# Kernel optimization log

Measured on AMD Instinct MI355X. Metric: run time of the kernel, lower is better.

Reference implementation:

```python
import jax, jax.numpy as jnp
import numpy as np

B, S, D, H = 4, 2048, 768, 8
HD = D // H
EPS = 1e-5
NEG = -1e9


def setup_inputs() -> dict:
    key = jax.random.key(0)
    ks = jax.random.split(key, 12)
    s = 1.0 / np.sqrt(D)
    inp = {
        "hidden_states": jax.random.normal(ks[0], (B, S, D), dtype=jnp.float32),
        "anchor_mask": jax.random.bernoulli(ks[1], 0.5, (B, S)),
        "ln_g": jnp.ones((D,), jnp.float32),
        "ln_b": jnp.zeros((D,), jnp.float32),
        "Wq": jax.random.uniform(ks[2], (D, D), jnp.float32, -s, s),
        "bq": jax.random.uniform(ks[3], (D,), jnp.float32, -s, s),
        "Wk": jax.random.uniform(ks[4], (D, D), jnp.float32, -s, s),
        "bk": jax.random.uniform(ks[5], (D,), jnp.float32, -s, s),
        "Wv": jax.random.uniform(ks[6], (D, D), jnp.float32, -s, s),
        "bv": jax.random.uniform(ks[7], (D,), jnp.float32, -s, s),
        "Wo": jax.random.uniform(ks[8], (D, D), jnp.float32, -s, s),
        "bo": jax.random.uniform(ks[9], (D,), jnp.float32, -s, s),
    }
    return inp


def reference(hidden_states, anchor_mask, ln_g, ln_b, Wq, bq, Wk, bk, Wv, bv, Wo, bo):
    # LayerNorm (per-token, so applying to all tokens == applying to gathered anchors)
    mu = jnp.mean(hidden_states, axis=-1, keepdims=True)
    var = jnp.mean(jnp.square(hidden_states - mu), axis=-1, keepdims=True)
    x = (hidden_states - mu) * jax.lax.rsqrt(var + EPS) * ln_g + ln_b

    # QKV projections: torch Linear is x @ W.T + b
    q = (jnp.einsum('bsd,ed->bse', x, Wq) + bq).reshape(B, S, H, HD)
    k = (jnp.einsum('bsd,ed->bse', x, Wk) + bk).reshape(B, S, H, HD)
    v = (jnp.einsum('bsd,ed->bse', x, Wv) + bv).reshape(B, S, H, HD)

    scale = 1.0 / np.sqrt(HD)
    scores = jnp.einsum('bqhd,bkhd->bhqk', q, k) * scale
    # keys restricted to anchor positions (equivalent to the gather)
    key_mask = anchor_mask[:, None, None, :]  # (B,1,1,S)
    scores = jnp.where(key_mask, scores, NEG)
    attn = jax.nn.softmax(scores, axis=-1)  # dropout is identity in eval

    out = jnp.einsum('bhqk,bkhd->bqhd', attn, v).reshape(B, S, D)
    out = jnp.einsum('bsd,ed->bse', out, Wo) + bo
    # scatter back: zeros at non-anchor positions
    return out * anchor_mask[:, :, None].astype(out.dtype)
```

## Files before the change

### kernel.cpp

```cpp
#include <hip/hip_runtime.h>
#include <math.h>

#define S_LEN 2048
#define D_DIM 768
#define NH 8
#define HD 96
#define NTOK 8192

typedef short bf16x8 __attribute__((ext_vector_type(8)));
typedef float f32x4 __attribute__((ext_vector_type(4)));
typedef float f32x16 __attribute__((ext_vector_type(16)));
typedef unsigned int u32x2 __attribute__((ext_vector_type(2)));
typedef unsigned int u32x4 __attribute__((ext_vector_type(4)));

__device__ __forceinline__ f32x4 mfma16(bf16x8 a, bf16x8 b, f32x4 c) {
    return __builtin_amdgcn_mfma_f32_16x16x32_bf16(a, b, c, 0, 0, 0);
}
__device__ __forceinline__ f32x16 mfma32(bf16x8 a, bf16x8 b, f32x16 c) {
    return __builtin_amdgcn_mfma_f32_32x32x16_bf16(a, b, c, 0, 0, 0);
}

__device__ __forceinline__ unsigned short f2bf(float f) {
    unsigned int u = __float_as_uint(f);
    u += 0x7fffu + ((u >> 16) & 1u);
    return (unsigned short)(u >> 16);
}

__device__ __forceinline__ unsigned int cvtpk(float lo, float hi) {
    unsigned int r;
    asm("v_cvt_pk_bf16_f32 %0, %1, %2" : "=v"(r) : "v"(lo), "v"(hi));
    return r;
}

__device__ __forceinline__ void gl_lds16(const unsigned short* g, unsigned short* l) {
    __builtin_amdgcn_global_load_lds(
        (const __attribute__((address_space(1))) unsigned int*)g,
        (__attribute__((address_space(3))) unsigned int*)l, 16, 0, 0);
}

#define TILE_SHORTS 6144
#define BH_SHORTS   196608

__global__ __launch_bounds__(256) void prep_kernel(
    const unsigned char* __restrict__ mb, int* __restrict__ idx, int* __restrict__ cnt,
    const float* __restrict__ Wq, const float* __restrict__ Wk,
    const float* __restrict__ Wv, const float* __restrict__ Wo,
    unsigned short* __restrict__ W4b, float* __restrict__ out)
{
    const int bi = blockIdx.x;
    const int t  = threadIdx.x;

    if (bi < 4) {
        __shared__ int red[4];
        __shared__ int warp_tot[4];
        const int b = bi;
        int s = 0;
        for (int i = t; i < NTOK; i += 256) s += (int)mb[i];
        for (int off = 32; off > 0; off >>= 1) s += __shfl_down(s, off, 64);
        if ((t & 63) == 0) red[t >> 6] = s;
        __syncthreads();
        const int total = red[0] + red[1] + red[2] + red[3];
        const int mode = (total > 20000) ? 2 : ((total > 2500) ? 1 : 0);
        const int*   mi = (const int*)mb;
        const float* mf = (const float*)mb;
        const int p0 = t * 8;
        int av = 0, c = 0;
        #pragma unroll
        for (int j = 0; j < 8; ++j) {
            const int g = b * S_LEN + p0 + j;
            bool a;
            if (mode == 2)      a = (mf[g] != 0.0f);
            else if (mode == 1) a = (mb[g] != 0);
            else                a = (mi[g] != 0);
            if (a) { av |= (1 << j); ++c; }
        }
        const int lane = t & 63, w = t >> 6;
        int v = c;
        #pragma unroll
        for (int off = 1; off < 64; off <<= 1) {
            const int u = __shfl_up(v, off, 64);
            if (lane >= off) v += u;
        }
        if (lane == 63) warp_tot[w] = v;
        __syncthreads();
        int wbase = 0;
        for (int i = 0; i < w; ++i) wbase += warp_tot[i];
        int o = wbase + v - c;
        #pragma unroll
        for (int j = 0; j < 8; ++j)
            if (av & (1 << j)) idx[b * S_LEN + (o++)] = p0 + j;
        if (t == 255) cnt[b] = wbase + v;
    } else if (bi < 1156) {
        const int i = bi - 4;
        const int w = i / 288, blk = i % 288;
        const float* src = (w == 0) ? Wq : (w == 1) ? Wk : (w == 2) ? Wv : Wo;
        const int base = (blk * 256 + t) * 8;
        const float4 a = *(const float4*)&src[base];
        const float4 c = *(const float4*)&src[base + 4];
        uint4 u;
        u.x = (unsigned int)f2bf(a.x) | ((unsigned int)f2bf(a.y) << 16);
        u.y = (unsigned int)f2bf(a.z) | ((unsigned int)f2bf(a.w) << 16);
        u.z = (unsigned int)f2bf(c.x) | ((unsigned int)f2bf(c.y) << 16);
        u.w = (unsigned int)f2bf(c.z) | ((unsigned int)f2bf(c.w) << 16);
        *(uint4*)&W4b[(size_t)w * 589824 + base] = u;
    } else {
        const size_t i4 = (size_t)(bi - 1156) * 256 + t;
        float4 z; z.x = z.y = z.z = z.w = 0.0f;
        *(float4*)&out[i4 * 4] = z;
    }
}

__global__ __launch_bounds__(256) void ln_gather_kernel(
    const float* __restrict__ H, const float* __restrict__ g,
    const float* __restrict__ bta, const int* __restrict__ idx,
    const int* __restrict__ cnt, unsigned short* __restrict__ X)
{
    __shared__ float rs[4], rss[4];
    const int slot = blockIdx.x;
    const int b = slot >> 11, r = slot & (S_LEN - 1);
    if (r >= cnt[b]) return;
    const int p = idx[slot];
    const float* hr = H + (size_t)(b * S_LEN + p) * D_DIM;
    unsigned short* xr = X + (size_t)slot * D_DIM;
    const int t = threadIdx.x;
    const float v0 = hr[t], v1 = hr[t + 256], v2 = hr[t + 512];
    float s  = v0 + v1 + v2;
    float ss = v0*v0 + v1*v1 + v2*v2;
    for (int off = 32; off > 0; off >>= 1) {
        s  += __shfl_down(s,  off, 64);
        ss += __shfl_down(ss, off, 64);
    }
    if ((t & 63) == 0) { rs[t >> 6] = s; rss[t >> 6] = ss; }
    __syncthreads();
    const float sum = rs[0] + rs[1] + rs[2] + rs[3];
    const float sq  = rss[0] + rss[1] + rss[2] + rss[3];
    const float mu  = sum * (1.0f / D_DIM);
    const float var = sq * (1.0f / D_DIM) - mu * mu;
    const float rstd = rsqrtf(var + 1e-5f);
    xr[t]       = f2bf((v0 - mu) * rstd * g[t]       + bta[t]);
    xr[t + 256] = f2bf((v1 - mu) * rstd * g[t + 256] + bta[t + 256]);
    xr[t + 512] = f2bf((v2 - mu) * rstd * g[t + 512] + bta[t + 512]);
}

__global__ __launch_bounds__(256) void gemm_bf16(
    const unsigned short* __restrict__ A,
    const unsigned short* __restrict__ W4,
    const float* __restrict__ b0, const float* __restrict__ b1,
    const float* __restrict__ b2,
    const int* __restrict__ cnt, const int* __restrict__ idx,
    unsigned short* __restrict__ Qo, unsigned short* __restrict__ Kp,
    unsigned short* __restrict__ Vp, float* __restrict__ Fo,
    int oproj)
{
    const int z = blockIdx.z;
    const int m0 = blockIdx.y * 128;
    const int b  = m0 >> 11;
    const int rbase = m0 & (S_LEN - 1);
    const int nc = cnt[b];
    if (rbase >= nc) return;
    const int n0 = blockIdx.x * 128;
    const unsigned short* W = W4 + (size_t)z * 589824;
    const float* bias = (z == 0) ? b0 : (z == 1 ? b1 : b2);

    __shared__ unsigned short Al[128 * 32];
    __shared__ unsigned short Bl[128 * 32];

    const int t = threadIdx.x;
    const int srow = t >> 2, sg = t & 3;
    const int ra0 = b * S_LEN + min(rbase + srow,      nc - 1);
    const int ra1 = b * S_LEN + min(rbase + srow + 64, nc - 1);
    const unsigned short* gA0 = A + (size_t)ra0 * 768 + sg * 8;
    const unsigned short* gA1 = A + (size_t)ra1 * 768 + sg * 8;
    const unsigned short* gB0 = W + (size_t)(n0 + srow)      * 768 + sg * 8;
    const unsigned short* gB1 = W + (size_t)(n0 + srow + 64) * 768 + sg * 8;
    unsigned short* lA = Al + t * 8;
    unsigned short* lB = Bl + t * 8;

    const int w = t >> 6, lane = t & 63;
    const int l15 = lane & 15, quad = lane >> 4;
    const int mh = (w & 1) * 64, nh2 = (w >> 1) * 64;

    f32x4 acc[4][4] = {};

    int aoff[4], boff[4];
    #pragma unroll
    for (int i = 0; i < 4; ++i) {
        aoff[i] = (mh  + i * 16 + l15) * 32 + quad * 8;
        boff[i] = (nh2 + i * 16 + l15) * 32 + quad * 8;
    }

    for (int k0 = 0; k0 < 768; k0 += 32) {
        __syncthreads();
        gl_lds16(gA0 + k0, lA);
        gl_lds16(gA1 + k0, lA + 2048);
        gl_lds16(gB0 + k0, lB);
        gl_lds16(gB1 + k0, lB + 2048);
        __syncthreads();
        bf16x8 af[4], bfr[4];
        #pragma unroll
        for (int i = 0; i < 4; ++i) af[i]  = *(const bf16x8*)(Al + aoff[i]);
        #pragma unroll
        for (int i = 0; i < 4; ++i) bfr[i] = *(const bf16x8*)(Bl + boff[i]);
        #pragma unroll
        for (int ms = 0; ms < 4; ++ms)
            #pragma unroll
            for (int ns = 0; ns < 4; ++ns)
                acc[ms][ns] = mfma16(af[ms], bfr[ns], acc[ms][ns]);
    }

    if (!oproj) {
        if (z == 0) {
            #pragma unroll
            for (int ns = 0; ns < 4; ++ns) {
                const int n = n0 + nh2 + ns * 16 + l15;
                const float bv = bias[n];
                #pragma unroll
                for (int ms = 0; ms < 4; ++ms) {
                    const int ml = mh + ms * 16 + quad * 4;
                    #pragma unroll
                    for (int r = 0; r < 4; ++r) {
                        const int slot = b * S_LEN + rbase + ml + r;
                        Qo[(size_t)slot * 768 + n] = f2bf(acc[ms][ns][r] + bv);
                    }
                }
            }
        } else if (z == 1) {
            #pragma unroll
            for (int ns = 0; ns < 4; ++ns) {
                const int n = n0 + nh2 + ns * 16 + l15;
                const int h = n / 96, d = n - h * 96;
                const float bv = bias[n];
                unsigned short* base = Kp + (size_t)(b * 8 + h) * BH_SHORTS;
                const int dseg = d >> 3, dlo = d & 7;
                #pragma unroll
                for (int ms = 0; ms < 4; ++ms) {
                    const int ml = mh + ms * 16 + quad * 4;
                    #pragma unroll
                    for (int r = 0; r < 4; ++r) {
                        const int tok = rbase + ml + r;
                        const int kt = tok >> 6, tk = tok & 63;
                        const int g16 = tk >> 4, lr = tk & 15;
                        base[(size_t)kt * TILE_SHORTS +
                             (g16 * 192 + dseg * 16 + lr) * 8 + dlo] =
                            (tok < nc) ? f2bf(acc[ms][ns][r] + bv)
                                       : (unsigned short)0;
                    }
                }
            }
        } else {
            #pragma unroll
            for (int ns = 0; ns < 4; ++ns) {
                const int n = n0 + nh2 + ns * 16 + l15;
                const int h = n / 96, d = n - h * 96;
                const float bv = bias[n];
                unsigned short* base = Vp + (size_t)(b * 8 + h) * BH_SHORTS;
                const int dg = d >> 4, l16 = d & 15;
                #pragma unroll
                for (int ms = 0; ms < 4; ++ms) {
                    const int ml = mh + ms * 16 + quad * 4;
                    const int k = rbase + ml;
                    const int kt = k >> 6, tk = k & 63;
                    const int kseg = tk >> 3, klo = tk & 7;
                    const unsigned short h0 =
                        (k + 0 < nc) ? f2bf(acc[ms][ns][0] + bv) : (unsigned short)0;
                    const unsigned short h1 =
                        (k + 1 < nc) ? f2bf(acc[ms][ns][1] + bv) : (unsigned short)0;
                    const unsigned short h2 =
                        (k + 2 < nc) ? f2bf(acc[ms][ns][2] + bv) : (unsigned short)0;
                    const unsigned short h3 =
                        (k + 3 < nc) ? f2bf(acc[ms][ns][3] + bv) : (unsigned short)0;
                    uint2 u;
                    u.x = (unsigned int)h0 | ((unsigned int)h1 << 16);
                    u.y = (unsigned int)h2 | ((unsigned int)h3 << 16);
                    *(uint2*)&base[(size_t)kt * TILE_SHORTS +
                                   (dg * 128 + kseg * 16 + l16) * 8 + klo] = u;
                }
            }
        }
    } else {
        #pragma unroll
        for (int ns = 0; ns < 4; ++ns) {
            const int n = n0 + nh2 + ns * 16 + l15;
            const float bv = bias[n];
            #pragma unroll
            for (int ms = 0; ms < 4; ++ms) {
                const int ml = mh + ms * 16 + quad * 4;
                #pragma unroll
                for (int r = 0; r < 4; ++r) {
                    const int rloc = rbase + ml + r;
                    if (rloc < nc) {
                        const int orow = b * S_LEN + idx[b * S_LEN + rloc];
                        Fo[(size_t)orow * 768 + n] = acc[ms][ns][r] + bv;
                    }
                }
            }
        }
    }
}

__global__ __launch_bounds__(256) void attn_mfma(
    const unsigned short* __restrict__ Q,
    const unsigned short* __restrict__ Kp,
    const unsigned short* __restrict__ Vp,
    const int* __restrict__ cnt,
    unsigned short* __restrict__ O)
{
    const int bh = blockIdx.x & 31;
    const int b  = bh >> 3, h = bh & 7;
    const int q0 = (blockIdx.x >> 5) * 32;
    const int nk = cnt[b];
    if (q0 >= nk) return;

    __shared__ f32x4 CMB4[2][64][13];

    const int t = threadIdx.x, w = t >> 6, lane = t & 63;
    const int l15 = lane & 15;
    const int gh  = (lane >> 4) & 1;
    const int hi  = lane >> 5;
    const int q32 = lane & 31;
    const int bS  = b * S_LEN;
    const float CE = 0.14724459f;

    const unsigned short* Kg = Kp + (size_t)(b * 8 + h) * BH_SHORTS;
    const unsigned short* Vg = Vp + (size_t)(b * 8 + h) * BH_SHORTS;

    const unsigned short* qrow = Q + (size_t)(bS + q0 + q32) * 768 + h * 96 + hi * 8;
    bf16x8 qf[6];
    #pragma unroll
    for (int ks = 0; ks < 6; ++ks) qf[ks] = *(const bf16x8*)(qrow + ks * 16);

    const int kb0 = (gh * 192 + hi * 16 + l15) * 8;
    const int vb0 = (gh * 128 + hi * 16 + l15) * 8;

    float ls0 = 0.0f, ls1 = 0.0f;
    f32x16 oacc[3] = {};

    const int kts = (nk + 63) >> 6;

    for (int kt = w; kt < kts; kt += 4) {
        const unsigned short* Kt = Kg + (size_t)kt * TILE_SHORTS + kb0;
        const unsigned short* Vt = Vg + (size_t)kt * TILE_SHORTS + vb0;

        #pragma unroll
        for (int s = 0; s < 2; ++s) {
            bf16x8 kf[6];
            #pragma unroll
            for (int ks = 0; ks < 6; ++ks)
                kf[ks] = *(const bf16x8*)(Kt + (s * 384 + ks * 32) * 8);
            f32x16 sa = {};
            __builtin_amdgcn_s_setprio(1);
            #pragma unroll
            for (int ks = 0; ks < 6; ++ks) sa = mfma32(kf[ks], qf[ks], sa);
            __builtin_amdgcn_s_setprio(0);

            unsigned int wv[8];
            #pragma unroll
            for (int j = 0; j < 8; ++j) {
                const float e0 = exp2f(sa[2 * j]     * CE);
                const float e1 = exp2f(sa[2 * j + 1] * CE);
                if (j & 1) ls1 += e0 + e1; else ls0 += e0 + e1;
                wv[j] = cvtpk(e0, e1);
            }
            const u32x2 r02 = __builtin_amdgcn_permlane32_swap(wv[0], wv[2], false, false);
            const u32x2 r13 = __builtin_amdgcn_permlane32_swap(wv[1], wv[3], false, false);
            const u32x2 r46 = __builtin_amdgcn_permlane32_swap(wv[4], wv[6], false, false);
            const u32x2 r57 = __builtin_amdgcn_permlane32_swap(wv[5], wv[7], false, false);
            const u32x4 pw0 = { r02.x, r13.x, r02.y, r13.y };
            const u32x4 pw1 = { r46.x, r57.x, r46.y, r57.y };
            const bf16x8 pb0 = __builtin_bit_cast(bf16x8, pw0);
            const bf16x8 pb1 = __builtin_bit_cast(bf16x8, pw1);

            const int kkb = s * 2;
            __builtin_amdgcn_s_setprio(1);
            #pragma unroll
            for (int dg = 0; dg < 3; ++dg) {
                const bf16x8 v0 = *(const bf16x8*)(Vt + (dg * 256 + kkb * 32) * 8);
                const bf16x8 v1 = *(const bf16x8*)(Vt + (dg * 256 + (kkb + 1) * 32) * 8);
                oacc[dg] = mfma32(v0, pb0, oacc[dg]);
                oacc[dg] = mfma32(v1, pb1, oacc[dg]);
            }
            __builtin_amdgcn_s_setprio(0);
        }
    }

    float lsum = ls0 + ls1;
    lsum += __shfl_xor(lsum, 32);

    if (w >= 2) {
        f32x4* dst = CMB4[w - 2][lane];
        #pragma unroll
        for (int dg = 0; dg < 3; ++dg)
            #pragma unroll
            for (int m = 0; m < 4; ++m) {
                const f32x4 p = { oacc[dg][4 * m],     oacc[dg][4 * m + 1],
                                  oacc[dg][4 * m + 2], oacc[dg][4 * m + 3] };
                dst[dg * 4 + m] = p;
            }
        const f32x4 tl = { lsum, 0.0f, 0.0f, 0.0f };
        dst[12] = tl;
    }
    __syncthreads();
    if (w < 2) {
        const f32x4* src = CMB4[w][lane];
        #pragma unroll
        for (int dg = 0; dg < 3; ++dg)
            #pragma unroll
            for (int m = 0; m < 4; ++m) {
                const f32x4 p = src[dg * 4 + m];
                #pragma unroll
                for (int j = 0; j < 4; ++j) oacc[dg][4 * m + j] += p[j];
            }
        lsum += src[12][0];
    }
    __syncthreads();
    if (w == 1) {
        f32x4* dst = CMB4[0][lane];
        #pragma unroll
        for (int dg = 0; dg < 3; ++dg)
            #pragma unroll
            for (int m = 0; m < 4; ++m) {
                const f32x4 p = { oacc[dg][4 * m],     oacc[dg][4 * m + 1],
                                  oacc[dg][4 * m + 2], oacc[dg][4 * m + 3] };
                dst[dg * 4 + m] = p;
            }
        const f32x4 tl = { lsum, 0.0f, 0.0f, 0.0f };
        dst[12] = tl;
    }
    __syncthreads();
    if (w > 0) return;

    {
        const f32x4* src = CMB4[0][lane];
        #pragma unroll
        for (int dg = 0; dg < 3; ++dg)
            #pragma unroll
            for (int m = 0; m < 4; ++m) {
                const f32x4 p = src[dg * 4 + m];
                #pragma unroll
                for (int j = 0; j < 4; ++j) oacc[dg][4 * m + j] += p[j];
            }
        lsum += src[12][0];
    }
    lsum -= (float)((kts << 6) - nk);

    const int qi = q0 + q32;
    if (qi < nk) {
        const float rl = 1.0f / lsum;
        unsigned short* og = O + (size_t)(bS + qi) * 768 + h * 96;
        #pragma unroll
        for (int dg = 0; dg < 3; ++dg) {
            #pragma unroll
            for (int m = 0; m < 4; ++m) {
                uint2 u;
                u.x = cvtpk(oacc[dg][4 * m]     * rl, oacc[dg][4 * m + 1] * rl);
                u.y = cvtpk(oacc[dg][4 * m + 2] * rl, oacc[dg][4 * m + 3] * rl);
                *(uint2*)&og[dg * 32 + m * 8 + hi * 4] = u;
            }
        }
    }
}

extern "C" void kernel_launch(void* const* d_in, const int* in_sizes, int n_in,
                              void* d_out, int out_size, void* d_ws, size_t ws_size,
                              hipStream_t stream)
{
    const float* hs  = (const float*)d_in[0];
    const unsigned char* am = (const unsigned char*)d_in[1];
    const float* lng = (const float*)d_in[2];
    const float* lnb = (const float*)d_in[3];
    const float* Wq  = (const float*)d_in[4];
    const float* bq  = (const float*)d_in[5];
    const float* Wk  = (const float*)d_in[6];
    const float* bk  = (const float*)d_in[7];
    const float* Wv  = (const float*)d_in[8];
    const float* bv  = (const float*)d_in[9];
    const float* Wo  = (const float*)d_in[10];
    const float* bo  = (const float*)d_in[11];

    char* ws = (char*)d_ws;
    const size_t BUF = (size_t)NTOK * 768 * 2;
    int* idx = (int*)ws;
    int* cnt = (int*)(ws + 32768);
    unsigned short* xb  = (unsigned short*)(ws + 65536);
    unsigned short* Qb  = (unsigned short*)(ws + 65536 + BUF);
    unsigned short* Kpb = (unsigned short*)(ws + 65536 + 2 * BUF);
    unsigned short* Vpb = (unsigned short*)(ws + 65536 + 3 * BUF);
    unsigned short* W4b = (unsigned short*)(ws + 65536 + 4 * BUF);
    unsigned short* Ob  = xb;
    float* out = (float*)d_out;

    prep_kernel<<<dim3(2692), dim3(256), 0, stream>>>(
        am, idx, cnt, Wq, Wk, Wv, Wo, W4b, out);

    ln_gather_kernel<<<dim3(NTOK), dim3(256), 0, stream>>>(hs, lng, lnb, idx, cnt, xb);

    gemm_bf16<<<dim3(6, 64, 3), dim3(256), 0, stream>>>(
        xb, W4b, bq, bk, bv, cnt, idx, Qb, Kpb, Vpb, nullptr, 0);

    attn_mfma<<<dim3(2048), dim3(256), 0, stream>>>(Qb, Kpb, Vpb, cnt, Ob);

    gemm_bf16<<<dim3(6, 64, 1), dim3(256), 0, stream>>>(
        Ob, W4b + (size_t)3 * 589824, bo, bo, bo, cnt, idx,
        nullptr, nullptr, nullptr, out, 1);
}
```

Before: 196.2 us.

## Double-buffer GEMM LDS loads and merge two query tiles per attention block

The GEMM main loop now uses two LDS buffers, so the global-to-LDS copy for the next k-slice is issued before the MFMAs on the current one, and each iteration needs one barrier instead of two. The attention kernel now runs 512 threads per block covering 64 queries (two 32-query sets of four key-split waves each), halving the block count. This is meant to overlap memory latency with compute in the GEMM and cut per-block overhead in attention. In exchange it doubles GEMM LDS use and makes the attention blocks larger, which may reduce occupancy or load balance.

```diff
diff --git a/kernel.cpp b/kernel.cpp
--- a/kernel.cpp
+++ b/kernel.cpp
@@ -162,8 +162,8 @@
     const unsigned short* W = W4 + (size_t)z * 589824;
     const float* bias = (z == 0) ? b0 : (z == 1 ? b1 : b2);
 
-    __shared__ unsigned short Al[128 * 32];
-    __shared__ unsigned short Bl[128 * 32];
+    __shared__ unsigned short Al[2][128 * 32];
+    __shared__ unsigned short Bl[2][128 * 32];
 
     const int t = threadIdx.x;
     const int srow = t >> 2, sg = t & 3;
@@ -173,8 +173,7 @@
     const unsigned short* gA1 = A + (size_t)ra1 * 768 + sg * 8;
     const unsigned short* gB0 = W + (size_t)(n0 + srow)      * 768 + sg * 8;
     const unsigned short* gB1 = W + (size_t)(n0 + srow + 64) * 768 + sg * 8;
-    unsigned short* lA = Al + t * 8;
-    unsigned short* lB = Bl + t * 8;
+    const int t8 = t * 8;
 
     const int w = t >> 6, lane = t & 63;
     const int l15 = lane & 15, quad = lane >> 4;
@@ -189,23 +188,32 @@
         boff[i] = (nh2 + i * 16 + l15) * 32 + quad * 8;
     }
 
-    for (int k0 = 0; k0 < 768; k0 += 32) {
-        __syncthreads();
-        gl_lds16(gA0 + k0, lA);
-        gl_lds16(gA1 + k0, lA + 2048);
-        gl_lds16(gB0 + k0, lB);
-        gl_lds16(gB1 + k0, lB + 2048);
-        __syncthreads();
+    gl_lds16(gA0, &Al[0][t8]);
+    gl_lds16(gA1, &Al[0][2048 + t8]);
+    gl_lds16(gB0, &Bl[0][t8]);
+    gl_lds16(gB1, &Bl[0][2048 + t8]);
+    __syncthreads();
+
+    for (int it = 0; it < 24; ++it) {
+        const int cur = it & 1;
+        if (it + 1 < 24) {
+            const int k1 = (it + 1) * 32;
+            gl_lds16(gA0 + k1, &Al[cur ^ 1][t8]);
+            gl_lds16(gA1 + k1, &Al[cur ^ 1][2048 + t8]);
+            gl_lds16(gB0 + k1, &Bl[cur ^ 1][t8]);
+            gl_lds16(gB1 + k1, &Bl[cur ^ 1][2048 + t8]);
+        }
         bf16x8 af[4], bfr[4];
         #pragma unroll
-        for (int i = 0; i < 4; ++i) af[i]  = *(const bf16x8*)(Al + aoff[i]);
-        #pragma unroll
-        for (int i = 0; i < 4; ++i) bfr[i] = *(const bf16x8*)(Bl + boff[i]);
+        for (int i = 0; i < 4; ++i) af[i]  = *(const bf16x8*)(&Al[cur][aoff[i]]);
+        #pragma unroll
+        for (int i = 0; i < 4; ++i) bfr[i] = *(const bf16x8*)(&Bl[cur][boff[i]]);
         #pragma unroll
         for (int ms = 0; ms < 4; ++ms)
             #pragma unroll
             for (int ns = 0; ns < 4; ++ns)
                 acc[ms][ns] = mfma16(af[ms], bfr[ns], acc[ms][ns]);
+        __syncthreads();
     }
 
     if (!oproj) {
@@ -298,7 +306,7 @@
     }
 }
 
-__global__ __launch_bounds__(256) void attn_mfma(
+__global__ __launch_bounds__(512) void attn_mfma(
     const unsigned short* __restrict__ Q,
     const unsigned short* __restrict__ Kp,
     const unsigned short* __restrict__ Vp,
@@ -307,24 +315,26 @@
 {
     const int bh = blockIdx.x & 31;
     const int b  = bh >> 3, h = bh & 7;
-    const int q0 = (blockIdx.x >> 5) * 32;
+    const int q0 = (blockIdx.x >> 5) * 64;
     const int nk = cnt[b];
     if (q0 >= nk) return;
 
-    __shared__ f32x4 CMB4[2][64][13];
+    __shared__ f32x4 CMB4[2][2][64][13];
 
     const int t = threadIdx.x, w = t >> 6, lane = t & 63;
+    const int qset = w >> 2, kw = w & 3;
     const int l15 = lane & 15;
     const int gh  = (lane >> 4) & 1;
     const int hi  = lane >> 5;
     const int q32 = lane & 31;
+    const int qb  = q0 + qset * 32;
     const int bS  = b * S_LEN;
     const float CE = 0.14724459f;
 
     const unsigned short* Kg = Kp + (size_t)(b * 8 + h) * BH_SHORTS;
     const unsigned short* Vg = Vp + (size_t)(b * 8 + h) * BH_SHORTS;
 
-    const unsigned short* qrow = Q + (size_t)(bS + q0 + q32) * 768 + h * 96 + hi * 8;
+    const unsigned short* qrow = Q + (size_t)(bS + qb + q32) * 768 + h * 96 + hi * 8;
     bf16x8 qf[6];
     #pragma unroll
     for (int ks = 0; ks < 6; ++ks) qf[ks] = *(const bf16x8*)(qrow + ks * 16);
@@ -337,7 +347,7 @@
 
     const int kts = (nk + 63) >> 6;
 
-    for (int kt = w; kt < kts; kt += 4) {
+    for (int kt = kw; kt < kts; kt += 4) {
         const unsigned short* Kt = Kg + (size_t)kt * TILE_SHORTS + kb0;
         const unsigned short* Vt = Vg + (size_t)kt * TILE_SHORTS + vb0;
 
@@ -386,8 +396,8 @@
     float lsum = ls0 + ls1;
     lsum += __shfl_xor(lsum, 32);
 
-    if (w >= 2) {
-        f32x4* dst = CMB4[w - 2][lane];
+    if (kw >= 2) {
+        f32x4* dst = CMB4[qset][kw - 2][lane];
         #pragma unroll
         for (int dg = 0; dg < 3; ++dg)
             #pragma unroll
@@ -400,8 +410,8 @@
         dst[12] = tl;
     }
     __syncthreads();
-    if (w < 2) {
-        const f32x4* src = CMB4[w][lane];
+    if (kw < 2) {
+        const f32x4* src = CMB4[qset][kw][lane];
         #pragma unroll
         for (int dg = 0; dg < 3; ++dg)
             #pragma unroll
@@ -413,8 +423,8 @@
         lsum += src[12][0];
     }
     __syncthreads();
-    if (w == 1) {
-        f32x4* dst = CMB4[0][lane];
+    if (kw == 1) {
+        f32x4* dst = CMB4[qset][0][lane];
         #pragma unroll
         for (int dg = 0; dg < 3; ++dg)
             #pragma unroll
@@ -427,10 +437,10 @@
         dst[12] = tl;
     }
     __syncthreads();
-    if (w > 0) return;
+    if (kw != 0) return;
 
     {
-        const f32x4* src = CMB4[0][lane];
+        const f32x4* src = CMB4[qset][0][lane];
         #pragma unroll
         for (int dg = 0; dg < 3; ++dg)
             #pragma unroll
@@ -443,7 +453,7 @@
     }
     lsum -= (float)((kts << 6) - nk);
 
-    const int qi = q0 + q32;
+    const int qi = qb + q32;
     if (qi < nk) {
         const float rl = 1.0f / lsum;
         unsigned short* og = O + (size_t)(bS + qi) * 768 + h * 96;
@@ -497,7 +507,7 @@
     gemm_bf16<<<dim3(6, 64, 3), dim3(256), 0, stream>>>(
         xb, W4b, bq, bk, bv, cnt, idx, Qb, Kpb, Vpb, nullptr, 0);
 
-    attn_mfma<<<dim3(2048), dim3(256), 0, stream>>>(Qb, Kpb, Vpb, cnt, Ob);
+    attn_mfma<<<dim3(1024), dim3(512), 0, stream>>>(Qb, Kpb, Vpb, cnt, Ob);
 
     gemm_bf16<<<dim3(6, 64, 1), dim3(256), 0, stream>>>(
         Ob, W4b + (size_t)3 * 589824, bo, bo, bo, cnt, idx,
```

Result: slower. 213.3 us (+8.7%).

## Double-buffer GEMM LDS tiles, halve M-tile, prefetch K fragments in attention

Applied to the files above, without the earlier changes.

The GEMM now uses a 64x128 tile with double-buffered LDS, so the next k-slice's global-to-LDS load is issued before computing on the current slice. This needs one barrier per iteration instead of two, and the grid doubles to 128 row blocks. In attention, each wave loads the K fragments for the next sub-tile before doing the current QK MFMA to hide load latency. The cost is more registers from the prefetched fragments, less reuse per GEMM tile, and the risk of a hazard between the async LDS writes and the reads of the other buffer.

```diff
diff --git a/kernel.cpp b/kernel.cpp
--- a/kernel.cpp
+++ b/kernel.cpp
@@ -153,7 +153,7 @@
     int oproj)
 {
     const int z = blockIdx.z;
-    const int m0 = blockIdx.y * 128;
+    const int m0 = blockIdx.y * 64;
     const int b  = m0 >> 11;
     const int rbase = m0 & (S_LEN - 1);
     const int nc = cnt[b];
@@ -162,50 +162,53 @@
     const unsigned short* W = W4 + (size_t)z * 589824;
     const float* bias = (z == 0) ? b0 : (z == 1 ? b1 : b2);
 
-    __shared__ unsigned short Al[128 * 32];
-    __shared__ unsigned short Bl[128 * 32];
+    __shared__ unsigned short Al[2][64 * 32];
+    __shared__ unsigned short Bl[2][128 * 32];
 
     const int t = threadIdx.x;
     const int srow = t >> 2, sg = t & 3;
-    const int ra0 = b * S_LEN + min(rbase + srow,      nc - 1);
-    const int ra1 = b * S_LEN + min(rbase + srow + 64, nc - 1);
+    const int ra0 = b * S_LEN + min(rbase + srow, nc - 1);
     const unsigned short* gA0 = A + (size_t)ra0 * 768 + sg * 8;
-    const unsigned short* gA1 = A + (size_t)ra1 * 768 + sg * 8;
     const unsigned short* gB0 = W + (size_t)(n0 + srow)      * 768 + sg * 8;
     const unsigned short* gB1 = W + (size_t)(n0 + srow + 64) * 768 + sg * 8;
-    unsigned short* lA = Al + t * 8;
-    unsigned short* lB = Bl + t * 8;
+    const int t8 = t * 8;
 
     const int w = t >> 6, lane = t & 63;
     const int l15 = lane & 15, quad = lane >> 4;
-    const int mh = (w & 1) * 64, nh2 = (w >> 1) * 64;
-
-    f32x4 acc[4][4] = {};
-
-    int aoff[4], boff[4];
+    const int mh = (w & 1) * 32, nh2 = (w >> 1) * 64;
+
+    f32x4 acc[2][4] = {};
+
+    int aoff[2], boff[4];
     #pragma unroll
-    for (int i = 0; i < 4; ++i) {
-        aoff[i] = (mh  + i * 16 + l15) * 32 + quad * 8;
-        boff[i] = (nh2 + i * 16 + l15) * 32 + quad * 8;
-    }
-
-    for (int k0 = 0; k0 < 768; k0 += 32) {
-        __syncthreads();
-        gl_lds16(gA0 + k0, lA);
-        gl_lds16(gA1 + k0, lA + 2048);
-        gl_lds16(gB0 + k0, lB);
-        gl_lds16(gB1 + k0, lB + 2048);
-        __syncthreads();
-        bf16x8 af[4], bfr[4];
-        #pragma unroll
-        for (int i = 0; i < 4; ++i) af[i]  = *(const bf16x8*)(Al + aoff[i]);
-        #pragma unroll
-        for (int i = 0; i < 4; ++i) bfr[i] = *(const bf16x8*)(Bl + boff[i]);
-        #pragma unroll
-        for (int ms = 0; ms < 4; ++ms)
+    for (int i = 0; i < 2; ++i) aoff[i] = (mh  + i * 16 + l15) * 32 + quad * 8;
+    #pragma unroll
+    for (int i = 0; i < 4; ++i) boff[i] = (nh2 + i * 16 + l15) * 32 + quad * 8;
+
+    gl_lds16(gA0, &Al[0][t8]);
+    gl_lds16(gB0, &Bl[0][t8]);
+    gl_lds16(gB1, &Bl[0][2048 + t8]);
+    __syncthreads();
+
+    for (int it = 0; it < 24; ++it) {
+        const int cur = it & 1;
+        if (it + 1 < 24) {
+            const int k1 = (it + 1) * 32;
+            gl_lds16(gA0 + k1, &Al[cur ^ 1][t8]);
+            gl_lds16(gB0 + k1, &Bl[cur ^ 1][t8]);
+            gl_lds16(gB1 + k1, &Bl[cur ^ 1][2048 + t8]);
+        }
+        bf16x8 af[2], bfr[4];
+        #pragma unroll
+        for (int i = 0; i < 2; ++i) af[i]  = *(const bf16x8*)(&Al[cur][aoff[i]]);
+        #pragma unroll
+        for (int i = 0; i < 4; ++i) bfr[i] = *(const bf16x8*)(&Bl[cur][boff[i]]);
+        #pragma unroll
+        for (int ms = 0; ms < 2; ++ms)
             #pragma unroll
             for (int ns = 0; ns < 4; ++ns)
                 acc[ms][ns] = mfma16(af[ms], bfr[ns], acc[ms][ns]);
+        __syncthreads();
     }
 
     if (!oproj) {
@@ -215,7 +218,7 @@
                 const int n = n0 + nh2 + ns * 16 + l15;
                 const float bv = bias[n];
                 #pragma unroll
-                for (int ms = 0; ms < 4; ++ms) {
+                for (int ms = 0; ms < 2; ++ms) {
                     const int ml = mh + ms * 16 + quad * 4;
                     #pragma unroll
                     for (int r = 0; r < 4; ++r) {
@@ -233,7 +236,7 @@
                 unsigned short* base = Kp + (size_t)(b * 8 + h) * BH_SHORTS;
                 const int dseg = d >> 3, dlo = d & 7;
                 #pragma unroll
-                for (int ms = 0; ms < 4; ++ms) {
+                for (int ms = 0; ms < 2; ++ms) {
                     const int ml = mh + ms * 16 + quad * 4;
                     #pragma unroll
                     for (int r = 0; r < 4; ++r) {
@@ -256,7 +259,7 @@
                 unsigned short* base = Vp + (size_t)(b * 8 + h) * BH_SHORTS;
                 const int dg = d >> 4, l16 = d & 15;
                 #pragma unroll
-                for (int ms = 0; ms < 4; ++ms) {
+                for (int ms = 0; ms < 2; ++ms) {
                     const int ml = mh + ms * 16 + quad * 4;
                     const int k = rbase + ml;
                     const int kt = k >> 6, tk = k & 63;
@@ -283,7 +286,7 @@
             const int n = n0 + nh2 + ns * 16 + l15;
             const float bv = bias[n];
             #pragma unroll
-            for (int ms = 0; ms < 4; ++ms) {
+            for (int ms = 0; ms < 2; ++ms) {
                 const int ml = mh + ms * 16 + quad * 4;
                 #pragma unroll
                 for (int r = 0; r < 4; ++r) {
@@ -337,49 +340,64 @@
 
     const int kts = (nk + 63) >> 6;
 
-    for (int kt = w; kt < kts; kt += 4) {
-        const unsigned short* Kt = Kg + (size_t)kt * TILE_SHORTS + kb0;
-        const unsigned short* Vt = Vg + (size_t)kt * TILE_SHORTS + vb0;
-
-        #pragma unroll
-        for (int s = 0; s < 2; ++s) {
-            bf16x8 kf[6];
-            #pragma unroll
-            for (int ks = 0; ks < 6; ++ks)
-                kf[ks] = *(const bf16x8*)(Kt + (s * 384 + ks * 32) * 8);
-            f32x16 sa = {};
-            __builtin_amdgcn_s_setprio(1);
-            #pragma unroll
-            for (int ks = 0; ks < 6; ++ks) sa = mfma32(kf[ks], qf[ks], sa);
-            __builtin_amdgcn_s_setprio(0);
-
-            unsigned int wv[8];
-            #pragma unroll
-            for (int j = 0; j < 8; ++j) {
-                const float e0 = exp2f(sa[2 * j]     * CE);
-                const float e1 = exp2f(sa[2 * j + 1] * CE);
-                if (j & 1) ls1 += e0 + e1; else ls0 += e0 + e1;
-                wv[j] = cvtpk(e0, e1);
-            }
-            const u32x2 r02 = __builtin_amdgcn_permlane32_swap(wv[0], wv[2], false, false);
-            const u32x2 r13 = __builtin_amdgcn_permlane32_swap(wv[1], wv[3], false, false);
-            const u32x2 r46 = __builtin_amdgcn_permlane32_swap(wv[4], wv[6], false, false);
-            const u32x2 r57 = __builtin_amdgcn_permlane32_swap(wv[5], wv[7], false, false);
-            const u32x4 pw0 = { r02.x, r13.x, r02.y, r13.y };
-            const u32x4 pw1 = { r46.x, r57.x, r46.y, r57.y };
-            const bf16x8 pb0 = __builtin_bit_cast(bf16x8, pw0);
-            const bf16x8 pb1 = __builtin_bit_cast(bf16x8, pw1);
-
-            const int kkb = s * 2;
-            __builtin_amdgcn_s_setprio(1);
-            #pragma unroll
-            for (int dg = 0; dg < 3; ++dg) {
-                const bf16x8 v0 = *(const bf16x8*)(Vt + (dg * 256 + kkb * 32) * 8);
-                const bf16x8 v1 = *(const bf16x8*)(Vt + (dg * 256 + (kkb + 1) * 32) * 8);
-                oacc[dg] = mfma32(v0, pb0, oacc[dg]);
-                oacc[dg] = mfma32(v1, pb1, oacc[dg]);
-            }
-            __builtin_amdgcn_s_setprio(0);
+    if (w < kts) {
+        const unsigned short* Kt0 = Kg + (size_t)w * TILE_SHORTS + kb0;
+        bf16x8 kfc[6];
+        #pragma unroll
+        for (int ks = 0; ks < 6; ++ks)
+            kfc[ks] = *(const bf16x8*)(Kt0 + (ks * 32) * 8);
+
+        for (int kt = w; kt < kts; kt += 4) {
+            const unsigned short* Kt = Kg + (size_t)kt * TILE_SHORTS + kb0;
+            const unsigned short* Vt = Vg + (size_t)kt * TILE_SHORTS + vb0;
+
+            #pragma unroll
+            for (int s = 0; s < 2; ++s) {
+                const unsigned short* Kn = (s == 0)
+                    ? (Kt + 384 * 8)
+                    : (Kt + (size_t)4 * TILE_SHORTS);
+                bf16x8 kfn[6];
+                #pragma unroll
+                for (int ks = 0; ks < 6; ++ks)
+                    kfn[ks] = *(const bf16x8*)(Kn + (ks * 32) * 8);
+
+                f32x16 sa = {};
+                __builtin_amdgcn_s_setprio(1);
+                #pragma unroll
+                for (int ks = 0; ks < 6; ++ks) sa = mfma32(kfc[ks], qf[ks], sa);
+                __builtin_amdgcn_s_setprio(0);
+
+                unsigned int wv[8];
+                #pragma unroll
+                for (int j = 0; j < 8; ++j) {
+                    const float e0 = exp2f(sa[2 * j]     * CE);
+                    const float e1 = exp2f(sa[2 * j + 1] * CE);
+                    if (j & 1) ls1 += e0 + e1; else ls0 += e0 + e1;
+                    wv[j] = cvtpk(e0, e1);
+                }
+                const u32x2 r02 = __builtin_amdgcn_permlane32_swap(wv[0], wv[2], false, false);
+                const u32x2 r13 = __builtin_amdgcn_permlane32_swap(wv[1], wv[3], false, false);
+                const u32x2 r46 = __builtin_amdgcn_permlane32_swap(wv[4], wv[6], false, false);
+                const u32x2 r57 = __builtin_amdgcn_permlane32_swap(wv[5], wv[7], false, false);
+                const u32x4 pw0 = { r02.x, r13.x, r02.y, r13.y };
+                const u32x4 pw1 = { r46.x, r57.x, r46.y, r57.y };
+                const bf16x8 pb0 = __builtin_bit_cast(bf16x8, pw0);
+                const bf16x8 pb1 = __builtin_bit_cast(bf16x8, pw1);
+
+                const int kkb = s * 2;
+                __builtin_amdgcn_s_setprio(1);
+                #pragma unroll
+                for (int dg = 0; dg < 3; ++dg) {
+                    const bf16x8 v0 = *(const bf16x8*)(Vt + (dg * 256 + kkb * 32) * 8);
+                    const bf16x8 v1 = *(const bf16x8*)(Vt + (dg * 256 + (kkb + 1) * 32) * 8);
+                    oacc[dg] = mfma32(v0, pb0, oacc[dg]);
+                    oacc[dg] = mfma32(v1, pb1, oacc[dg]);
+                }
+                __builtin_amdgcn_s_setprio(0);
+
+                #pragma unroll
+                for (int ks = 0; ks < 6; ++ks) kfc[ks] = kfn[ks];
+            }
         }
     }
 
@@ -494,12 +512,12 @@
 
     ln_gather_kernel<<<dim3(NTOK), dim3(256), 0, stream>>>(hs, lng, lnb, idx, cnt, xb);
 
-    gemm_bf16<<<dim3(6, 64, 3), dim3(256), 0, stream>>>(
+    gemm_bf16<<<dim3(6, 128, 3), dim3(256), 0, stream>>>(
         xb, W4b, bq, bk, bv, cnt, idx, Qb, Kpb, Vpb, nullptr, 0);
 
     attn_mfma<<<dim3(2048), dim3(256), 0, stream>>>(Qb, Kpb, Vpb, cnt, Ob);
 
-    gemm_bf16<<<dim3(6, 64, 1), dim3(256), 0, stream>>>(
+    gemm_bf16<<<dim3(6, 128, 1), dim3(256), 0, stream>>>(
         Ob, W4b + (size_t)3 * 589824, bo, bo, bo, cnt, idx,
         nullptr, nullptr, nullptr, out, 1);
 }
```

Result: slower. 200.5 us (+2.2%).
